# Optimization experiments

Hardware: AMD Instinct MI355X
Metric: run time of the kernel (lower is better)

## Reference

```python
import jax, jax.numpy as jnp
import numpy as np

EMBED = 1024
HEADS = 16
HEAD_DIM = EMBED // HEADS
WINDOW = 1024
HALF = WINDOW // 2  # effective causal lookback per token is HALF (window positions > i are masked)
SCALE = HEAD_DIM ** -0.5
B, T = 2, 4096


def setup_inputs() -> dict:
    key = jax.random.key(0)
    ks = jax.random.split(key, 11)
    f = jnp.float32
    return {
        'query': jax.random.normal(ks[0], (B, T, EMBED), f),
        'key':   jax.random.normal(ks[1], (B, T, EMBED), f),
        'value': jax.random.normal(ks[2], (B, T, EMBED), f),
        'wq': jax.random.normal(ks[3], (EMBED, EMBED), f) * 0.02,
        'bq': jax.random.normal(ks[4], (EMBED,), f) * 0.02,
        'wk': jax.random.normal(ks[5], (EMBED, EMBED), f) * 0.02,
        'bk': jax.random.normal(ks[6], (EMBED,), f) * 0.02,
        'wv': jax.random.normal(ks[7], (EMBED, EMBED), f) * 0.02,
        'bv': jax.random.normal(ks[8], (EMBED,), f) * 0.02,
        'wo': jax.random.normal(ks[9], (EMBED, EMBED), f) * 0.02,
        'bo': jax.random.normal(ks[10], (EMBED,), f) * 0.02,
    }


def _sliding_window_attn(q, k, v):
    # q,k,v: [B,H,T,D]; each query i attends to keys j with i-HALF <= j <= i.
    # Blocked formulation with block size Bk=HALF: block b attends to blocks b-1 and b.
    Bq, H, Tq, D = q.shape
    Bk = HALF
    nb = Tq // Bk  # T chosen to be a multiple of HALF
    qb = q.reshape(Bq, H, nb, Bk, D)

    def ctx(x):
        xb = x.reshape(Bq, H, nb, Bk, D)
        prev = jnp.concatenate([jnp.zeros_like(xb[:, :, :1]), xb[:, :, :-1]], axis=2)
        return jnp.concatenate([prev, xb], axis=3)  # [B,H,nb,2Bk,D]

    kc, vc = ctx(k), ctx(v)
    scores = jnp.einsum('bhnrd,bhncd->bhnrc', qb, kc)  # [B,H,nb,Bk,2Bk]
    r = jnp.arange(Bk)[:, None]          # query pos within block
    c = jnp.arange(2 * Bk)[None, :]      # key pos within [prev|cur] context
    # global diff = (Bk + r) - c; valid iff 0 <= diff <= HALF  <=>  r <= c <= r + Bk
    band = (c >= r) & (c <= r + Bk)      # [Bk, 2Bk]
    b_idx = jnp.arange(nb)[:, None, None]
    valid = band[None] & ((b_idx > 0) | (c[None] >= Bk))  # first block has no prev keys
    neg_inf = jnp.finfo(jnp.float32).min
    scores = jnp.where(valid[None, None], scores.astype(jnp.float32), neg_inf)
    attn = jax.nn.softmax(scores, axis=-1).astype(q.dtype)
    out = jnp.einsum('bhnrc,bhncd->bhnrd', attn, vc)
    return out.reshape(Bq, H, Tq, D)


def reference(query, key, value, wq, bq, wk, bk, wv, bv, wo, bo):
    Bq, Tq, C = query.shape
    split = lambda x: x.reshape(Bq, Tq, HEADS, HEAD_DIM).transpose(0, 2, 1, 3)
    q = split(jnp.einsum('btc,oc->bto', query, wq) + bq) * SCALE
    k = split(jnp.einsum('btc,oc->bto', key, wk) + bk)
    v = split(jnp.einsum('btc,oc->bto', value, wv) + bv)
    o = _sliding_window_attn(q, k, v)                       # [B,H,T,D]
    o = o.transpose(0, 2, 1, 3).reshape(Bq, Tq, C)
    return jnp.einsum('btc,oc->bto', o, wo) + bo
```

## Files before the change

### kernel.cpp

```cpp
#include <hip/hip_runtime.h>
#include <hip/hip_bf16.h>

typedef __attribute__((ext_vector_type(8))) short short8;
typedef __attribute__((ext_vector_type(4))) float f32x4;

__device__ __forceinline__ unsigned short f2bf(float f) {
  union { float f; unsigned int u; } x; x.f = f;
  unsigned int r = x.u + 0x7fffu + ((x.u >> 16) & 1u);
  return (unsigned short)(r >> 16);
}

__device__ __forceinline__ float fexp2(float x) {
#if __has_builtin(__builtin_amdgcn_exp2f)
  return __builtin_amdgcn_exp2f(x);
#else
  float r;
  asm("v_exp_f32 %0, %1" : "=v"(r) : "v"(x));
  return r;
#endif
}

#define MFMA16(a, b, c) __builtin_amdgcn_mfma_f32_16x16x32_bf16((a), (b), (c), 0, 0, 0)

__device__ __forceinline__ void gload_lds16(const void* g, void* l) {
  __builtin_amdgcn_global_load_lds((const __attribute__((address_space(1))) void*)g,
                                   (__attribute__((address_space(3))) void*)l, 16, 0, 0);
}

#define WAIT_VM(n) asm volatile("s_waitcnt vmcnt(" #n ")" ::: "memory")
#define RAW_BAR() asm volatile("s_barrier" ::: "memory")

__device__ __forceinline__ void p32swap(unsigned int& a, unsigned int& b) {
  asm volatile("v_permlane32_swap_b32 %0, %1" : "+v"(a), "+v"(b));
}
__device__ __forceinline__ void p16swap(unsigned int& a, unsigned int& b) {
  asm volatile("v_permlane16_swap_b32 %0, %1" : "+v"(a), "+v"(b));
}

#define QSCALE 0.1803368801111244f

__global__ __launch_bounds__(256) void cvt_all(
    const float* __restrict__ q, const float* __restrict__ k,
    const float* __restrict__ v, const float* __restrict__ w0,
    const float* __restrict__ w1, const float* __restrict__ w2,
    const float* __restrict__ w3, unsigned short* __restrict__ Tb,
    unsigned short* __restrict__ Kc, unsigned short* __restrict__ Vc,
    unsigned short* __restrict__ Wb) {
  const int lin = blockIdx.x;
  const float* src;
  unsigned short* dst;
  int i0;
  if (lin < 4096)        { src = q;  dst = Tb;                i0 = lin; }
  else if (lin < 8192)   { src = k;  dst = Kc;                i0 = lin - 4096; }
  else if (lin < 12288)  { src = v;  dst = Vc;                i0 = lin - 8192; }
  else if (lin < 12800)  { src = w0; dst = Wb;                i0 = lin - 12288; }
  else if (lin < 13312)  { src = w1; dst = Wb + (1u << 20);   i0 = lin - 12800; }
  else if (lin < 13824)  { src = w2; dst = Wb + (2u << 20);   i0 = lin - 13312; }
  else                   { src = w3; dst = Wb + (3u << 20);   i0 = lin - 13824; }
  const size_t i = (size_t)i0 * 256 + threadIdx.x;
  const float4* p = (const float4*)src + 2 * i;
  float4 a = p[0], b = p[1];
  ushort4 lo, hi;
  lo.x = f2bf(a.x); lo.y = f2bf(a.y); lo.z = f2bf(a.z); lo.w = f2bf(a.w);
  hi.x = f2bf(b.x); hi.y = f2bf(b.y); hi.z = f2bf(b.z); hi.w = f2bf(b.w);
  ((ushort4*)dst)[2 * i] = lo;
  ((ushort4*)dst)[2 * i + 1] = hi;
}

template <int MODE>
__global__ __launch_bounds__(512) void proj_gemm(const unsigned short* __restrict__ A,
                                                 const unsigned short* __restrict__ W,
                                                 const float* __restrict__ bias,
                                                 void* __restrict__ outp) {
  __shared__ unsigned short As[2][128 * 64];
  __shared__ unsigned short Bs[2][128 * 64];
  const int tid = threadIdx.x, lane = tid & 63, wid = tid >> 6;
  const int g = lane >> 4, li = lane & 15;
  const int wr = wid >> 1, wc = wid & 1;
  const int bm = blockIdx.x, bn = blockIdx.y;
  const int trow = tid >> 3;
  const int js = (tid & 7) ^ (trow & 7);

  f32x4 acc[2][4] = {};

  auto stage = [&](int kt, int pb) {
    const int k0 = kt << 6;
    #pragma unroll
    for (int r = 0; r < 2; ++r) {
      const int row = r * 64 + trow;
      gload_lds16(A + (size_t)(bm * 128 + row) * 1024 + k0 + js * 8,
                  &As[pb][(r * 64 + wid * 8) * 64]);
      gload_lds16(W + (size_t)(bn * 128 + row) * 1024 + k0 + js * 8,
                  &Bs[pb][(r * 64 + wid * 8) * 64]);
    }
  };

  stage(0, 0);
  int p = 0;
  for (int kt = 0; kt < 16; ++kt) {
    if (kt < 15) {
      stage(kt + 1, p ^ 1);
      WAIT_VM(4);
    } else {
      WAIT_VM(0);
    }
    RAW_BAR();
    #pragma unroll
    for (int kst = 0; kst < 2; ++kst) {
      short8 a[2], b[4];
      #pragma unroll
      for (int mi = 0; mi < 2; ++mi) {
        const int row = wr * 32 + mi * 16 + li;
        a[mi] = *(const short8*)((const char*)&As[p][0] + row * 128 +
                                 (((kst * 4 + g) ^ (li & 7)) << 4));
      }
      #pragma unroll
      for (int ni = 0; ni < 4; ++ni) {
        const int row = wc * 64 + ni * 16 + li;
        b[ni] = *(const short8*)((const char*)&Bs[p][0] + row * 128 +
                                 (((kst * 4 + g) ^ (li & 7)) << 4));
      }
      __builtin_amdgcn_s_setprio(1);
      #pragma unroll
      for (int mi = 0; mi < 2; ++mi)
        #pragma unroll
        for (int ni = 0; ni < 4; ++ni) {
          if constexpr (MODE == 2)
            acc[mi][ni] = MFMA16(b[ni], a[mi], acc[mi][ni]);
          else
            acc[mi][ni] = MFMA16(a[mi], b[ni], acc[mi][ni]);
        }
      __builtin_amdgcn_s_setprio(0);
    }
    RAW_BAR();
    p ^= 1;
  }

  #pragma unroll
  for (int mi = 0; mi < 2; ++mi) {
    #pragma unroll
    for (int ni = 0; ni < 4; ++ni) {
      if constexpr (MODE == 2) {
        const int mm = bm * 128 + wr * 32 + mi * 16 + li;
        const int b_ = mm >> 12, t_ = mm & 4095;
        #pragma unroll
        for (int r = 0; r < 4; ++r) {
          const int nn = bn * 128 + wc * 64 + ni * 16 + g * 4 + r;
          const int h_ = nn >> 6, d_ = nn & 63;
          float v = acc[mi][ni][r] + bias[nn];
          ((unsigned short*)outp)[(((size_t)(b_ * 16 + h_) * 64 + d_) << 12) + t_] = f2bf(v);
        }
      } else {
        const int nn = bn * 128 + wc * 64 + ni * 16 + li;
        const float bv_ = bias[nn];
        #pragma unroll
        for (int r = 0; r < 4; ++r) {
          const int mm = bm * 128 + wr * 32 + mi * 16 + g * 4 + r;
          float v = acc[mi][ni][r] + bv_;
          if constexpr (MODE == 0) v *= QSCALE;
          if constexpr (MODE <= 1) {
            const int b_ = mm >> 12, t_ = mm & 4095, h_ = nn >> 6, d_ = nn & 63;
            ((unsigned short*)outp)[(((size_t)(b_ * 16 + h_) * 4096 + t_) << 6) + d_] = f2bf(v);
          } else {
            ((float*)outp)[(size_t)mm * 1024 + nn] = v;
          }
        }
      }
    }
  }
}

__global__ __launch_bounds__(256) void swa_attn(const unsigned short* __restrict__ Q,
                                                const unsigned short* __restrict__ K,
                                                const unsigned short* __restrict__ V,
                                                unsigned short* __restrict__ O) {
  __shared__ unsigned short Kb[2][4096];
  __shared__ unsigned short Vb[2][4096];
  const int tid = threadIdx.x, lane = tid & 63, w = tid >> 6;
  const int g = lane >> 4, li = lane & 15;
  const int lin = blockIdx.x;
  const int xcd = lin & 7;
  const int rest = lin >> 3;
  const int qoff = rest & 7;
  const int grp = rest >> 3;
  const int G = xcd * 16 + grp;
  const int hb = G & 31;
  const int qb = (G >> 5) * 8 + qoff;
  const int qs = qb << 7;
  const int h = hb & 15, b = hb >> 4;
  const int bh = b * 16 + h;
  const unsigned short* Qh = Q + ((size_t)bh << 18);
  const unsigned short* Kh = K + ((size_t)bh << 18);
  const unsigned short* Vh = V + ((size_t)bh << 18);

  short8 qa[2][2];
  #pragma unroll
  for (int qt = 0; qt < 2; ++qt)
    #pragma unroll
    for (int kst = 0; kst < 2; ++kst)
      qa[qt][kst] =
          *(const short8*)&Qh[((size_t)(qs + w * 32 + qt * 16 + li) << 6) + kst * 32 + g * 8];

  const short8 vone = {0x3F80, 0x3F80, 0x3F80, 0x3F80, 0x3F80, 0x3F80, 0x3F80, 0x3F80};
  f32x4 o[2][4] = {};
  f32x4 lac[2] = {};
  const int c0 = (qs >= 512) ? 0 : ((512 - qs) >> 6);

  const int srow_hi = lane >> 3;
  const int sj = lane & 7;

  auto stage = [&](int c, int pb) {
    const int ks = qs - 512 + (c << 6);
    #pragma unroll
    for (int i = 0; i < 2; ++i) {
      const int seg = w + i * 4;
      const int row = seg * 8 + srow_hi;
      const int jsw = sj ^ (row & 7);
      gload_lds16(Kh + (((size_t)(ks + row)) << 6) + jsw * 8, &Kb[pb][seg * 512]);
      gload_lds16(Vh + (((size_t)row) << 12) + ks + jsw * 8, &Vb[pb][seg * 512]);
    }
  };

  int p = 0;
  stage(c0, 0);

  for (int c = c0; c <= 9; ++c) {
    if (c < 9) {
      stage(c + 1, p ^ 1);
      WAIT_VM(4);
    } else {
      WAIT_VM(0);
    }
    RAW_BAR();
    const int cb = c << 6;
    const bool anyq = (cb + 63 >= w * 32) && (cb <= w * 32 + 543);
    if (anyq) {
      short8 kf[4][2], vf[4][2];
      #pragma unroll
      for (int nt = 0; nt < 4; ++nt) {
        const int row = nt * 16 + li, rx = li & 7;
        #pragma unroll
        for (int kst = 0; kst < 2; ++kst) {
          const int byt = row * 128 + (((kst * 4 + g) ^ rx) << 4);
          kf[nt][kst] = *(const short8*)((const char*)&Kb[p][0] + byt);
          vf[nt][kst] = *(const short8*)((const char*)&Vb[p][0] + byt);
        }
      }
      #pragma unroll
      for (int qt = 0; qt < 2; ++qt) {
        const int base = w * 32 + qt * 16;
        if (cb + 63 < base || cb > base + 527) continue;
        f32x4 s[4];
        __builtin_amdgcn_s_setprio(1);
        #pragma unroll
        for (int nt = 0; nt < 4; ++nt) {
          f32x4 z = {};
          s[nt] = MFMA16(kf[nt][0], qa[qt][0], z);
          s[nt] = MFMA16(kf[nt][1], qa[qt][1], s[nt]);
        }
        __builtin_amdgcn_s_setprio(0);
        if (cb < base + 16 || cb + 63 > base + 512) {
          #pragma unroll
          for (int nt = 0; nt < 4; ++nt)
            #pragma unroll
            for (int r = 0; r < 4; ++r) {
              const int t1 = cb + nt * 16 + g * 4 + r - base;
              if (t1 < li || t1 > 512 + li) s[nt][r] = -3e38f;
            }
        }
        unsigned int pw[4][2];
        #pragma unroll
        for (int nt = 0; nt < 4; ++nt) {
          float2 ab; ab.x = fexp2(s[nt][0]); ab.y = fexp2(s[nt][1]);
          float2 cd; cd.x = fexp2(s[nt][2]); cd.y = fexp2(s[nt][3]);
          union { __hip_bfloat162 h2; unsigned int u; } u0, u1;
          u0.h2 = __float22bfloat162_rn(ab);
          u1.h2 = __float22bfloat162_rn(cd);
          pw[nt][0] = u0.u;
          pw[nt][1] = u1.u;
        }
        short8 pbf[2];
        #pragma unroll
        for (int kst = 0; kst < 2; ++kst) {
          unsigned int A0 = pw[2 * kst][0], B0 = pw[2 * kst + 1][0];
          unsigned int A1 = pw[2 * kst][1], B1 = pw[2 * kst + 1][1];
          p32swap(A0, B0);
          p32swap(A1, B1);
          p16swap(A0, B0);
          p16swap(A1, B1);
          union { unsigned int u[4]; short8 s8; } pb_;
          pb_.u[0] = A0;
          pb_.u[1] = A1;
          pb_.u[2] = B0;
          pb_.u[3] = B1;
          pbf[kst] = pb_.s8;
        }
        __builtin_amdgcn_s_setprio(1);
        lac[qt] = MFMA16(vone, pbf[0], lac[qt]);
        lac[qt] = MFMA16(vone, pbf[1], lac[qt]);
        #pragma unroll
        for (int dt = 0; dt < 4; ++dt) {
          o[qt][dt] = MFMA16(vf[dt][0], pbf[0], o[qt][dt]);
          o[qt][dt] = MFMA16(vf[dt][1], pbf[1], o[qt][dt]);
        }
        __builtin_amdgcn_s_setprio(0);
      }
    }
    RAW_BAR();
    p ^= 1;
  }

  #pragma unroll
  for (int qt = 0; qt < 2; ++qt) {
    const float inv = 1.0f / lac[qt][0];
    const int t_ = qs + w * 32 + qt * 16 + li;
    #pragma unroll
    for (int dt = 0; dt < 4; ++dt) {
      ushort4 u;
      u.x = f2bf(o[qt][dt][0] * inv); u.y = f2bf(o[qt][dt][1] * inv);
      u.z = f2bf(o[qt][dt][2] * inv); u.w = f2bf(o[qt][dt][3] * inv);
      *(ushort4*)&O[((size_t)(b * 4096 + t_) << 10) + h * 64 + dt * 16 + g * 4] = u;
    }
  }
}

extern "C" void kernel_launch(void* const* d_in, const int* in_sizes, int n_in,
                              void* d_out, int out_size, void* d_ws, size_t ws_size,
                              hipStream_t stream) {
  const float* q_in = (const float*)d_in[0];
  const float* k_in = (const float*)d_in[1];
  const float* v_in = (const float*)d_in[2];
  const float* wq = (const float*)d_in[3];
  const float* bq = (const float*)d_in[4];
  const float* wk = (const float*)d_in[5];
  const float* bk = (const float*)d_in[6];
  const float* wv = (const float*)d_in[7];
  const float* bv = (const float*)d_in[8];
  const float* wo = (const float*)d_in[9];
  const float* bo = (const float*)d_in[10];

  unsigned short* Qw = (unsigned short*)d_ws;
  unsigned short* Kw = Qw + (size_t)8388608;
  unsigned short* Vw = Kw + (size_t)8388608;
  unsigned short* Tb = Vw + (size_t)8388608;
  unsigned short* Wb = Tb + (size_t)8388608;
  unsigned short* Kc = (unsigned short*)d_out;
  unsigned short* Vc = Kc + (size_t)8388608;

  dim3 bb(256), bg(512), gg(64, 8);
  cvt_all<<<14336, bb, 0, stream>>>(q_in, k_in, v_in, wq, wk, wv, wo,
                                    Tb, Kc, Vc, Wb);
  proj_gemm<0><<<gg, bg, 0, stream>>>(Tb, Wb, bq, Qw);
  proj_gemm<1><<<gg, bg, 0, stream>>>(Kc, Wb + (1u << 20), bk, Kw);
  proj_gemm<2><<<gg, bg, 0, stream>>>(Vc, Wb + (2u << 20), bv, Vw);
  swa_attn<<<1024, bb, 0, stream>>>(Qw, Kw, Vw, Tb);
  proj_gemm<3><<<gg, bg, 0, stream>>>(Tb, Wb + (3u << 20), bo, (float*)d_out);
}
```

Measured before the change: 157.8 us.

## Load K/V fragments directly from global into registers, drop LDS staging

Removes the shared-memory double buffer and block barriers from the sliding-window attention kernel. Each wave now loads its K and V MFMA fragments straight from global memory into registers, software-pipelined one chunk ahead. It also trims each wave's chunk range to the chunks its queries actually need. This removes LDS traffic and barrier synchronisation, but the four waves in a block no longer share K/V data, so global/L2 traffic rises and register pressure grows.

```diff
diff --git a/kernel.cpp b/kernel.cpp
--- a/kernel.cpp
+++ b/kernel.cpp
@@ -174,8 +174,6 @@
                                                 const unsigned short* __restrict__ K,
                                                 const unsigned short* __restrict__ V,
                                                 unsigned short* __restrict__ O) {
-  __shared__ unsigned short Kb[2][4096];
-  __shared__ unsigned short Vb[2][4096];
   const int tid = threadIdx.x, lane = tid & 63, w = tid >> 6;
   const int g = lane >> 4, li = lane & 15;
   const int lin = blockIdx.x;
@@ -204,110 +202,105 @@
   const short8 vone = {0x3F80, 0x3F80, 0x3F80, 0x3F80, 0x3F80, 0x3F80, 0x3F80, 0x3F80};
   f32x4 o[2][4] = {};
   f32x4 lac[2] = {};
-  const int c0 = (qs >= 512) ? 0 : ((512 - qs) >> 6);
-
-  const int srow_hi = lane >> 3;
-  const int sj = lane & 7;
-
-  auto stage = [&](int c, int pb) {
+
+  int clo = (qs >= 512) ? 0 : ((512 - qs) >> 6);
+  const int wlo = (w >= 2) ? 1 : 0;
+  clo = (clo > wlo) ? clo : wlo;
+  const int chi = (w >= 2) ? 9 : 8;
+
+  auto loadK = [&](int c, short8 (&kf)[4][2]) {
     const int ks = qs - 512 + (c << 6);
     #pragma unroll
-    for (int i = 0; i < 2; ++i) {
-      const int seg = w + i * 4;
-      const int row = seg * 8 + srow_hi;
-      const int jsw = sj ^ (row & 7);
-      gload_lds16(Kh + (((size_t)(ks + row)) << 6) + jsw * 8, &Kb[pb][seg * 512]);
-      gload_lds16(Vh + (((size_t)row) << 12) + ks + jsw * 8, &Vb[pb][seg * 512]);
-    }
+    for (int nt = 0; nt < 4; ++nt)
+      #pragma unroll
+      for (int kst = 0; kst < 2; ++kst)
+        kf[nt][kst] =
+            *(const short8*)&Kh[((size_t)(ks + nt * 16 + li) << 6) + kst * 32 + g * 8];
   };
-
-  int p = 0;
-  stage(c0, 0);
-
-  for (int c = c0; c <= 9; ++c) {
-    if (c < 9) {
-      stage(c + 1, p ^ 1);
-      WAIT_VM(4);
-    } else {
-      WAIT_VM(0);
-    }
-    RAW_BAR();
+  auto loadV = [&](int c, short8 (&vf)[4][2]) {
+    const int ks = qs - 512 + (c << 6);
+    #pragma unroll
+    for (int dt = 0; dt < 4; ++dt)
+      #pragma unroll
+      for (int kst = 0; kst < 2; ++kst)
+        vf[dt][kst] =
+            *(const short8*)&Vh[(((size_t)(dt * 16 + li)) << 12) + ks + kst * 32 + g * 8];
+  };
+
+  auto compute = [&](int c, short8 (&kf)[4][2], short8 (&vf)[4][2]) {
     const int cb = c << 6;
-    const bool anyq = (cb + 63 >= w * 32) && (cb <= w * 32 + 543);
-    if (anyq) {
-      short8 kf[4][2], vf[4][2];
+    #pragma unroll
+    for (int qt = 0; qt < 2; ++qt) {
+      const int base = w * 32 + qt * 16;
+      if (cb + 63 < base || cb > base + 527) continue;
+      f32x4 s[4];
+      __builtin_amdgcn_s_setprio(1);
       #pragma unroll
       for (int nt = 0; nt < 4; ++nt) {
-        const int row = nt * 16 + li, rx = li & 7;
+        f32x4 z = {};
+        s[nt] = MFMA16(kf[nt][0], qa[qt][0], z);
+        s[nt] = MFMA16(kf[nt][1], qa[qt][1], s[nt]);
+      }
+      __builtin_amdgcn_s_setprio(0);
+      if (cb < base + 16 || cb + 63 > base + 512) {
         #pragma unroll
-        for (int kst = 0; kst < 2; ++kst) {
-          const int byt = row * 128 + (((kst * 4 + g) ^ rx) << 4);
-          kf[nt][kst] = *(const short8*)((const char*)&Kb[p][0] + byt);
-          vf[nt][kst] = *(const short8*)((const char*)&Vb[p][0] + byt);
-        }
-      }
-      #pragma unroll
-      for (int qt = 0; qt < 2; ++qt) {
-        const int base = w * 32 + qt * 16;
-        if (cb + 63 < base || cb > base + 527) continue;
-        f32x4 s[4];
-        __builtin_amdgcn_s_setprio(1);
-        #pragma unroll
-        for (int nt = 0; nt < 4; ++nt) {
-          f32x4 z = {};
-          s[nt] = MFMA16(kf[nt][0], qa[qt][0], z);
-          s[nt] = MFMA16(kf[nt][1], qa[qt][1], s[nt]);
-        }
-        __builtin_amdgcn_s_setprio(0);
-        if (cb < base + 16 || cb + 63 > base + 512) {
+        for (int nt = 0; nt < 4; ++nt)
           #pragma unroll
-          for (int nt = 0; nt < 4; ++nt)
-            #pragma unroll
-            for (int r = 0; r < 4; ++r) {
-              const int t1 = cb + nt * 16 + g * 4 + r - base;
-              if (t1 < li || t1 > 512 + li) s[nt][r] = -3e38f;
-            }
-        }
-        unsigned int pw[4][2];
-        #pragma unroll
-        for (int nt = 0; nt < 4; ++nt) {
-          float2 ab; ab.x = fexp2(s[nt][0]); ab.y = fexp2(s[nt][1]);
-          float2 cd; cd.x = fexp2(s[nt][2]); cd.y = fexp2(s[nt][3]);
-          union { __hip_bfloat162 h2; unsigned int u; } u0, u1;
-          u0.h2 = __float22bfloat162_rn(ab);
-          u1.h2 = __float22bfloat162_rn(cd);
-          pw[nt][0] = u0.u;
-          pw[nt][1] = u1.u;
-        }
-        short8 pbf[2];
-        #pragma unroll
-        for (int kst = 0; kst < 2; ++kst) {
-          unsigned int A0 = pw[2 * kst][0], B0 = pw[2 * kst + 1][0];
-          unsigned int A1 = pw[2 * kst][1], B1 = pw[2 * kst + 1][1];
-          p32swap(A0, B0);
-          p32swap(A1, B1);
-          p16swap(A0, B0);
-          p16swap(A1, B1);
-          union { unsigned int u[4]; short8 s8; } pb_;
-          pb_.u[0] = A0;
-          pb_.u[1] = A1;
-          pb_.u[2] = B0;
-          pb_.u[3] = B1;
-          pbf[kst] = pb_.s8;
-        }
-        __builtin_amdgcn_s_setprio(1);
-        lac[qt] = MFMA16(vone, pbf[0], lac[qt]);
-        lac[qt] = MFMA16(vone, pbf[1], lac[qt]);
-        #pragma unroll
-        for (int dt = 0; dt < 4; ++dt) {
-          o[qt][dt] = MFMA16(vf[dt][0], pbf[0], o[qt][dt]);
-          o[qt][dt] = MFMA16(vf[dt][1], pbf[1], o[qt][dt]);
-        }
-        __builtin_amdgcn_s_setprio(0);
-      }
-    }
-    RAW_BAR();
-    p ^= 1;
+          for (int r = 0; r < 4; ++r) {
+            const int t1 = cb + nt * 16 + g * 4 + r - base;
+            if (t1 < li || t1 > 512 + li) s[nt][r] = -3e38f;
+          }
+      }
+      unsigned int pw[4][2];
+      #pragma unroll
+      for (int nt = 0; nt < 4; ++nt) {
+        float2 ab; ab.x = fexp2(s[nt][0]); ab.y = fexp2(s[nt][1]);
+        float2 cd; cd.x = fexp2(s[nt][2]); cd.y = fexp2(s[nt][3]);
+        union { __hip_bfloat162 h2; unsigned int u; } u0, u1;
+        u0.h2 = __float22bfloat162_rn(ab);
+        u1.h2 = __float22bfloat162_rn(cd);
+        pw[nt][0] = u0.u;
+        pw[nt][1] = u1.u;
+      }
+      short8 pbf[2];
+      #pragma unroll
+      for (int kst = 0; kst < 2; ++kst) {
+        unsigned int A0 = pw[2 * kst][0], B0 = pw[2 * kst + 1][0];
+        unsigned int A1 = pw[2 * kst][1], B1 = pw[2 * kst + 1][1];
+        p32swap(A0, B0);
+        p32swap(A1, B1);
+        p16swap(A0, B0);
+        p16swap(A1, B1);
+        union { unsigned int u[4]; short8 s8; } pb_;
+        pb_.u[0] = A0;
+        pb_.u[1] = A1;
+        pb_.u[2] = B0;
+        pb_.u[3] = B1;
+        pbf[kst] = pb_.s8;
+      }
+      __builtin_amdgcn_s_setprio(1);
+      lac[qt] = MFMA16(vone, pbf[0], lac[qt]);
+      lac[qt] = MFMA16(vone, pbf[1], lac[qt]);
+      #pragma unroll
+      for (int dt = 0; dt < 4; ++dt) {
+        o[qt][dt] = MFMA16(vf[dt][0], pbf[0], o[qt][dt]);
+        o[qt][dt] = MFMA16(vf[dt][1], pbf[1], o[qt][dt]);
+      }
+      __builtin_amdgcn_s_setprio(0);
+    }
+  };
+
+  short8 kA[4][2], kB[4][2], vv[4][2];
+  loadK(clo, kA);
+  for (int c = clo; c <= chi; c += 2) {
+    loadV(c, vv);
+    if (c + 1 <= chi) loadK(c + 1, kB);
+    compute(c, kA, vv);
+    if (c + 1 <= chi) {
+      loadV(c + 1, vv);
+      if (c + 2 <= chi) loadK(c + 2, kA);
+      compute(c + 1, kB, vv);
+    }
   }
 
   #pragma unroll
```

After: 180.9 us. 1.15x slower.
